# Performance work log

Measured on AMD Instinct MI355X. Metric: run time of the kernel, lower is better.

The kernel has to match this reference:

```python
import jax, jax.numpy as jnp
import numpy as np
import math

B, T, D, H = 8, 1024, 512, 8
DK = D // H


def setup_inputs() -> dict:
    key = jax.random.key(0)
    ks = jax.random.split(key, 16)
    f = lambda k, s: jax.random.normal(k, s, dtype=jnp.float32)
    p = lambda k, s: jax.random.normal(k, s, dtype=jnp.float32) * 0.02
    return {
        "query": f(ks[0], (B, T, D)),
        "key": f(ks[1], (B, T, D)),
        "value": f(ks[2], (B, T, D)),
        "pos_embedding": f(ks[3], (B, T, D)),
        "Wq": p(ks[4], (D, D)), "bq": p(ks[5], (D,)),
        "Wk": p(ks[6], (D, D)), "bk": p(ks[7], (D,)),
        "Wv": p(ks[8], (D, D)), "bv": p(ks[9], (D,)),
        "Wp": p(ks[10], (D, D)),
        "u_bias": p(ks[11], (H, DK)),
        "v_bias": p(ks[12], (H, DK)),
        "Wo": p(ks[13], (D, D)), "bo": p(ks[14], (D,)),
    }


def _rel_shift(pos_score):
    # pos_score: [B, H, T, T]  -> Transformer-XL relative shift via pad/reshape
    b, h, t1, t2 = pos_score.shape
    padded = jnp.concatenate(
        [jnp.zeros((b, h, t1, 1), pos_score.dtype), pos_score], axis=-1
    )  # [B,H,T,T+1]
    padded = padded.reshape(b, h, t2 + 1, t1)
    return padded[:, :, 1:].reshape(b, h, t1, t2)


def reference(query, key, value, pos_embedding, Wq, bq, Wk, bk, Wv, bv, Wp,
              u_bias, v_bias, Wo, bo):
    q = (query @ Wq + bq).reshape(B, T, H, DK)          # [B,T,H,DK]
    k = (key @ Wk + bk).reshape(B, T, H, DK)
    v = (value @ Wv + bv).reshape(B, T, H, DK)
    p = (pos_embedding @ Wp).reshape(B, T, H, DK)

    content_score = jnp.einsum("bihd,bjhd->bhij", q + u_bias, k)
    pos_score = jnp.einsum("bihd,bjhd->bhij", q + v_bias, p)
    pos_score = _rel_shift(pos_score)

    score = (content_score + pos_score) / math.sqrt(D)  # note: sqrt(d_model)
    attn = jax.nn.softmax(score, axis=-1)               # dropout: eval mode
    context = jnp.einsum("bhij,bjhd->bihd", attn, v).reshape(B, T, D)
    return context @ Wo + bo
```

## Files before the change

### kernel.cpp

```cpp
#include <hip/hip_runtime.h>

#define B_ 8
#define T_ 1024
#define D_ 512
#define H_ 8
#define DK_ 64

typedef __bf16 bf16x8 __attribute__((ext_vector_type(8)));
typedef float f32x4 __attribute__((ext_vector_type(4)));

#define MFMA16(a, b, c) __builtin_amdgcn_mfma_f32_16x16x32_bf16(a, b, c, 0, 0, 0)

__device__ __forceinline__ bf16x8 pack8(float4 a, float4 b) {
  bf16x8 r;
  r[0] = (__bf16)a.x; r[1] = (__bf16)a.y; r[2] = (__bf16)a.z; r[3] = (__bf16)a.w;
  r[4] = (__bf16)b.x; r[5] = (__bf16)b.y; r[6] = (__bf16)b.z; r[7] = (__bf16)b.w;
  return r;
}

__device__ __forceinline__ void load_lds16(const void* g, void* l) {
  __builtin_amdgcn_global_load_lds(
      (const __attribute__((address_space(1))) void*)g,
      (__attribute__((address_space(3))) void*)l, 16, 0, 0);
}

__global__ __launch_bounds__(256) void cvt_w(const float* __restrict__ w0,
                                             const float* __restrict__ w1,
                                             const float* __restrict__ w2,
                                             const float* __restrict__ w3,
                                             const float* __restrict__ w4,
                                             __bf16* __restrict__ wt) {
  __shared__ float Ts[64][65];
  const float* W = (blockIdx.z == 0) ? w0
                 : (blockIdx.z == 1) ? w1
                 : (blockIdx.z == 2) ? w2
                 : (blockIdx.z == 3) ? w3 : w4;
  const int tid = threadIdx.x;
  const int kt = blockIdx.x * 64, nt = blockIdx.y * 64;
  const int r = tid >> 2, co = (tid & 3) * 16;
#pragma unroll
  for (int q = 0; q < 4; ++q)
    *(float4*)&Ts[r][co + q * 4] =
        *(const float4*)(W + (size_t)(kt + r) * 512 + nt + co + q * 4);
  __syncthreads();
  bf16x8 o0, o1;
#pragma unroll
  for (int q = 0; q < 8; ++q) o0[q] = (__bf16)Ts[co + q][r];
#pragma unroll
  for (int q = 0; q < 8; ++q) o1[q] = (__bf16)Ts[co + 8 + q][r];
  const int key = r & 7;
  __bf16* dst =
      wt + (size_t)blockIdx.z * 262144 + (size_t)(nt + r) * 512 + kt;
  *(bf16x8*)(dst + (((co >> 3) ^ key) << 3)) = o0;
  *(bf16x8*)(dst + ((((co >> 3) + 1) ^ key) << 3)) = o1;
}

template <int PHASE>
__global__ __launch_bounds__(256, 4) void gemm_dma(
    const float* __restrict__ qf, const float* __restrict__ kf,
    const float* __restrict__ vf, const float* __restrict__ pf,
    const __bf16* __restrict__ ctxA, const __bf16* __restrict__ Wt,
    const float* __restrict__ bq, const float* __restrict__ bk,
    const float* __restrict__ bv, const float* __restrict__ bo,
    const float* __restrict__ ub, const float* __restrict__ vb,
    __bf16* __restrict__ quB, __bf16* __restrict__ qvB,
    __bf16* __restrict__ kB, __bf16* __restrict__ vT,
    __bf16* __restrict__ pB, float* __restrict__ out) {
  __shared__ __bf16 smem[17408];
  __bf16* As = smem;
  __bf16* Bs = smem + 8192;
  const int tid = threadIdx.x;
  const int z = blockIdx.z;
  const int wave = tid >> 6, lane = tid & 63, l16 = lane & 15, quad = lane >> 4;
  const int wm = wave & 1, wn = wave >> 1;
  const int m0 = blockIdx.x * 128, n0 = blockIdx.y * 128;

  const float* Af = (z == 0) ? qf : (z == 1) ? kf : (z == 2) ? vf : pf;
  const __bf16* Bg = Wt + (size_t)(PHASE ? 4 : z) * (512 * 512);

  const int drow = tid >> 3, dch = (tid & 7) * 8;
  char* ldsA = (char*)As + (tid & 192) * 16;
  char* ldsB = (char*)Bs + (tid & 192) * 16;
  const int keyc = l16 & 7;

  f32x4 acc[4][4];
#pragma unroll
  for (int rb = 0; rb < 4; ++rb)
#pragma unroll
    for (int cb = 0; cb < 4; ++cb) acc[rb][cb] = 0.f;

#pragma unroll 1
  for (int k0 = 0; k0 < 512; k0 += 64) {
    __syncthreads();
#pragma unroll
    for (int c4 = 0; c4 < 4; ++c4)
      load_lds16(Bg + (size_t)(n0 + c4 * 32 + drow) * 512 + k0 + dch,
                 ldsB + c4 * 4096);
    if (PHASE == 1) {
#pragma unroll
      for (int c4 = 0; c4 < 4; ++c4)
        load_lds16(ctxA + (size_t)(m0 + c4 * 32 + drow) * 512 + k0 + dch,
                   ldsA + c4 * 4096);
    } else {
#pragma unroll
      for (int c4 = 0; c4 < 4; ++c4) {
        const int row = c4 * 32 + drow;
        const float* s = Af + (size_t)(m0 + row) * 512 + k0 + dch;
        float4 a0 = *(const float4*)s;
        float4 a1 = *(const float4*)(s + 4);
        *(bf16x8*)&As[row * 64 + ((((dch >> 3) ^ row) & 7) << 3)] =
            pack8(a0, a1);
      }
    }
    __syncthreads();
#pragma unroll
    for (int s = 0; s < 2; ++s) {
      const int ph = ((s * 4 + quad) ^ keyc) << 3;
      bf16x8 afr[4], bfr[4];
#pragma unroll
      for (int rb = 0; rb < 4; ++rb)
        afr[rb] = *(const bf16x8*)&As[(wm * 64 + rb * 16 + l16) * 64 + ph];
#pragma unroll
      for (int cb = 0; cb < 4; ++cb)
        bfr[cb] = *(const bf16x8*)&Bs[(wn * 64 + cb * 16 + l16) * 64 + ph];
#pragma unroll
      for (int rb = 0; rb < 4; ++rb)
#pragma unroll
        for (int cb = 0; cb < 4; ++cb)
          acc[rb][cb] = MFMA16(afr[rb], bfr[cb], acc[rb][cb]);
    }
  }

  if (PHASE == 1) {
#pragma unroll
    for (int rb = 0; rb < 4; ++rb)
#pragma unroll
      for (int cb = 0; cb < 4; ++cb) {
        const int col = n0 + wn * 64 + cb * 16 + l16;
        const float bb = bo[col];
#pragma unroll
        for (int r = 0; r < 4; ++r) {
          const int row = m0 + wm * 64 + rb * 16 + quad * 4 + r;
          out[(size_t)row * 512 + col] = acc[rb][cb][r] + bb;
        }
      }
    return;
  }

  __syncthreads();

  if (z == 2) {
    __bf16* Tt = smem;
#pragma unroll
    for (int rb = 0; rb < 4; ++rb)
#pragma unroll
      for (int cb = 0; cb < 4; ++cb) {
        const int cl = wn * 64 + cb * 16 + l16;
        const float bb = bv[n0 + cl];
#pragma unroll
        for (int r = 0; r < 4; ++r) {
          const int rl = wm * 64 + rb * 16 + quad * 4 + r;
          Tt[cl * 136 + rl] = (__bf16)(acc[rb][cb][r] + bb);
        }
      }
    __syncthreads();
    const int r2 = tid >> 1, ch = (tid & 1) * 64;
    const int hh = (n0 + r2) >> 6, dkk = (n0 + r2) & 63;
    const int bI = m0 >> 10, t0 = m0 & 1023;
    __bf16* dst = vT + (((size_t)(bI * H_ + hh)) * DK_ + dkk) * T_ + t0 + ch;
    const int vkey = dkk & 7;
#pragma unroll
    for (int q = 0; q < 8; ++q)
      *(bf16x8*)(dst + ((q ^ vkey) * 8)) =
          *(const bf16x8*)&Tt[r2 * 136 + ch + q * 8];
    return;
  }

  __bf16* Tt = smem;
  const int trow = tid & 127, hs = tid >> 7;
  const int bI = m0 >> 10, tt = (m0 & 1023) + trow;
  const int hh = (n0 >> 6) + hs;
  const size_t obase = (((size_t)(bI * H_ + hh)) * T_ + tt) * DK_;
  const int npass = (z == 0) ? 2 : 1;
#pragma unroll 1
  for (int pass = 0; pass < npass; ++pass) {
#pragma unroll
    for (int rb = 0; rb < 4; ++rb)
#pragma unroll
      for (int cb = 0; cb < 4; ++cb) {
        const int cl = wn * 64 + cb * 16 + l16;
        const int col = n0 + cl;
        const float b0 = (z == 0) ? bq[col] : (z == 1) ? bk[col] : 0.f;
        const float b1 = (z == 0) ? (pass ? vb[col] : ub[col]) : 0.f;
#pragma unroll
        for (int r = 0; r < 4; ++r) {
          const int rl = wm * 64 + rb * 16 + quad * 4 + r;
          Tt[rl * 136 + cl] = (__bf16)((acc[rb][cb][r] + b0) + b1);
        }
      }
    __syncthreads();
    __bf16* dst = ((z == 0) ? (pass ? qvB : quB) : (z == 1) ? kB : pB) + obase;
#pragma unroll
    for (int qd = 0; qd < 8; ++qd) {
      const int c = (z == 0) ? qd : (qd ^ (tt & 7));
      *(bf16x8*)(dst + c * 8) =
          *(const bf16x8*)&Tt[trow * 136 + hs * 64 + qd * 8];
    }
    if (pass + 1 < npass) __syncthreads();
  }
}

__global__ __launch_bounds__(256, 4) void attn_mfma(
    const __bf16* __restrict__ qu, const __bf16* __restrict__ qv,
    const __bf16* __restrict__ kbuf, const __bf16* __restrict__ vT,
    const __bf16* __restrict__ pbuf, __bf16* __restrict__ ctx) {
  constexpr float SCALE = 0.044194173824159216f;
  __shared__ __bf16 smemA[4488];
  __shared__ __bf16 Vt[4096];
  __shared__ __bf16 Pb[8192];
  __bf16* Kt = smemA;
  __bf16* Rs = smemA;
  __bf16* Pa = Pb;

  const int tid = threadIdx.x;
  const int wave = tid >> 6, lane = tid & 63, l16 = lane & 15, quad = lane >> 4;
  const int g = blockIdx.x;
  const int bhq = (g & 7) * 8 + (g >> 7);
  const int i0 = ((g >> 3) & 15) * 64;
  const size_t bh = (size_t)bhq * T_ * DK_;
  const __bf16* QU = qu + bh;
  const __bf16* QV = qv + bh;
  const __bf16* Kg = kbuf + bh;
  const __bf16* Vg = vT + bh;
  const __bf16* Pg = pbuf + bh;

  bf16x8 quA[2], qvw[2], qv4[2];
  {
    const int rw = i0 + wave * 16 + l16;
    const int r4g = i0 + 64 + l16;
    const int r4 = (r4g < T_) ? r4g : T_ - 1;
#pragma unroll
    for (int s = 0; s < 2; ++s) {
      const int ko = s * 32 + quad * 8;
      quA[s] = *(const bf16x8*)&QU[(size_t)rw * DK_ + ko];
      qvw[s] = *(const bf16x8*)&QV[(size_t)rw * DK_ + ko];
      qv4[s] = *(const bf16x8*)&QV[(size_t)r4 * DK_ + ko];
    }
  }

  f32x4 Oacc[4];
#pragma unroll
  for (int cb = 0; cb < 4; ++cb) Oacc[cb] = 0.f;
  float lrun[4];
#pragma unroll
  for (int r = 0; r < 4; ++r) lrun[r] = 0.f;

  const int rbase = wave * 16 + quad * 4;
  const int keyr = l16 & 7;
  const int keyp = (l16 + 7) & 7;
  const int drow = tid >> 3;
  const int dch = (tid & 7) * 8;
  char* ldsK = (char*)Kt + (tid & 192) * 16;
  char* ldsV = (char*)Vt + (tid & 192) * 16;
  char* ldsP = (char*)Pb + (tid & 192) * 16;

#pragma unroll 1
  for (int jt = 0; jt < 16; ++jt) {
    const int j0 = jt * 64;
    int cs = T_ - 65 + j0 - i0;
    if (cs < 0) cs += T_;
    if (cs >= T_) cs -= T_;

    __syncthreads();
    load_lds16(Kg + (size_t)(j0 + drow) * 64 + dch, ldsK);
    load_lds16(Kg + (size_t)(j0 + 32 + drow) * 64 + dch, ldsK + 4096);
    __builtin_amdgcn_sched_barrier(0);
    load_lds16(Vg + (size_t)drow * T_ + j0 + dch, ldsV);
    load_lds16(Vg + (size_t)(32 + drow) * T_ + j0 + dch, ldsV + 4096);
#pragma unroll
    for (int c = 0; c < 4; ++c) {
      int prow = cs + c * 32 + drow;
      if (prow >= T_) prow -= T_;
      load_lds16(Pg + (size_t)prow * 64 + dch, ldsP + c * 4096);
    }
    asm volatile("s_waitcnt vmcnt(6)" ::: "memory");
    __builtin_amdgcn_s_barrier();

    f32x4 sA[4];
#pragma unroll
    for (int cb = 0; cb < 4; ++cb) sA[cb] = 0.f;
#pragma unroll
    for (int s = 0; s < 2; ++s)
#pragma unroll
      for (int cb = 0; cb < 4; ++cb) {
        bf16x8 kf = *(const bf16x8*)&Kt[(cb * 16 + l16) * 64 +
                                        (((s * 4 + quad) ^ keyr) << 3)];
        sA[cb] = MFMA16(quA[s], kf, sA[cb]);
      }

    asm volatile("s_waitcnt vmcnt(0)" ::: "memory");
    __builtin_amdgcn_s_barrier();

#pragma unroll
    for (int c = 0; c < 5; ++c) {
      const int cb = 3 - wave + c;
      f32x4 rc = 0.f;
#pragma unroll
      for (int s = 0; s < 2; ++s) {
        bf16x8 pf = *(const bf16x8*)&Pb[(cb * 16 + l16) * 64 +
                                        (((s * 4 + quad) ^ keyp) << 3)];
        rc = MFMA16(qvw[s], pf, rc);
      }
      const int col = cb * 16 + l16;
#pragma unroll
      for (int rr = 0; rr < 4; ++rr) {
        const int dj = col + rbase + rr - 64;
        if (dj >= 0 && dj < 64) Rs[(rbase + rr) * 68 + dj] = (__bf16)rc[rr];
      }
    }
    {
      const int cb = wave;
      f32x4 rc = 0.f;
#pragma unroll
      for (int s = 0; s < 2; ++s) {
        bf16x8 pf = *(const bf16x8*)&Pb[(cb * 16 + l16) * 64 +
                                        (((s * 4 + quad) ^ keyp) << 3)];
        rc = MFMA16(qv4[s], pf, rc);
      }
      if (quad == 0) Rs[64 * 68 + cb * 16 + l16] = (__bf16)rc[0];
    }
    __syncthreads();

#pragma unroll
    for (int r = 0; r < 4; ++r) {
#pragma unroll
      for (int cb = 0; cb < 4; ++cb) {
        const int di = rbase + r;
        const int dj = cb * 16 + l16;
        const int ji = (j0 + dj) - (i0 + di);
        float pos = 0.f;
        if (ji != 1) pos = (float)Rs[(di + (ji >= 2 ? 1 : 0)) * 68 + dj];
        const float w_ = __expf((sA[cb][r] + pos) * SCALE);
        lrun[r] += w_;
        Pa[di * 64 + (dj & 7) + ((((dj >> 3) ^ di) & 7) << 3)] = (__bf16)w_;
      }
    }

#pragma unroll
    for (int s = 0; s < 2; ++s) {
      bf16x8 ap = *(const bf16x8*)&Pa[(wave * 16 + l16) * 64 +
                                      (((s * 4 + quad) ^ keyr) << 3)];
#pragma unroll
      for (int cb = 0; cb < 4; ++cb) {
        bf16x8 bv = *(const bf16x8*)&Vt[(cb * 16 + l16) * 64 +
                                        (((s * 4 + quad) ^ keyr) << 3)];
        Oacc[cb] = MFMA16(ap, bv, Oacc[cb]);
      }
    }
  }

  float inv[4];
#pragma unroll
  for (int r = 0; r < 4; ++r) {
    float L = lrun[r];
    L += __shfl_xor(L, 1);
    L += __shfl_xor(L, 2);
    L += __shfl_xor(L, 4);
    L += __shfl_xor(L, 8);
    inv[r] = 1.f / L;
  }
  const int b = bhq >> 3, h = bhq & 7;
#pragma unroll
  for (int cb = 0; cb < 4; ++cb)
#pragma unroll
    for (int r = 0; r < 4; ++r) {
      const int row = i0 + rbase + r;
      const int chunk = cb * 2 + (l16 >> 3);
      const int col = h * DK_ + ((chunk ^ (row & 7)) << 3) + (l16 & 7);
      ctx[((size_t)(b * T_ + row)) * D_ + col] = (__bf16)(Oacc[cb][r] * inv[r]);
    }
}

extern "C" void kernel_launch(void* const* d_in, const int* in_sizes, int n_in,
                              void* d_out, int out_size, void* d_ws,
                              size_t ws_size, hipStream_t stream) {
  const float* query = (const float*)d_in[0];
  const float* key   = (const float*)d_in[1];
  const float* value = (const float*)d_in[2];
  const float* pos   = (const float*)d_in[3];
  const float* Wq = (const float*)d_in[4];
  const float* bq = (const float*)d_in[5];
  const float* Wk = (const float*)d_in[6];
  const float* bk = (const float*)d_in[7];
  const float* Wv = (const float*)d_in[8];
  const float* bv = (const float*)d_in[9];
  const float* Wp = (const float*)d_in[10];
  const float* ub = (const float*)d_in[11];
  const float* vbias = (const float*)d_in[12];
  const float* Wo = (const float*)d_in[13];
  const float* bo = (const float*)d_in[14];
  float* out = (float*)d_out;

  char* ws = (char*)d_ws;
  const size_t ACT = (size_t)8192 * 512 * 2;
  __bf16* quB = (__bf16*)ws;
  __bf16* qvB = (__bf16*)(ws + 1 * ACT);
  __bf16* kB  = (__bf16*)(ws + 2 * ACT);
  __bf16* pB  = (__bf16*)(ws + 3 * ACT);
  __bf16* vT  = (__bf16*)(ws + 4 * ACT);
  __bf16* ctx = (__bf16*)(ws + 5 * ACT);
  __bf16* Wt  = (__bf16*)(ws + 6 * ACT);

  cvt_w<<<dim3(8, 8, 5), 256, 0, stream>>>(Wq, Wk, Wv, Wp, Wo, Wt);

  gemm_dma<0><<<dim3(64, 4, 4), 256, 0, stream>>>(
      query, key, value, pos, nullptr, Wt, bq, bk, bv, bo, ub, vbias,
      quB, qvB, kB, vT, pB, nullptr);

  attn_mfma<<<dim3(1024), 256, 0, stream>>>(quB, qvB, kB, vT, pB, ctx);

  gemm_dma<1><<<dim3(64, 4, 1), 256, 0, stream>>>(
      nullptr, nullptr, nullptr, nullptr, ctx, Wt, bq, bk, bv, bo, ub, vbias,
      quB, qvB, kB, vT, pB, out);
}
```

Before: 247.1 us.

## Double-buffer LDS tiles in projection GEMM to overlap loads with MFMA

Converts the projection/output GEMM main loop to a two-stage LDS double buffer. The next K-tile's global loads (DMA into LDS for weights and ctx, registers for the fp32 activations) are issued before the current tile's MFMAs and written afterwards, which removes one barrier per iteration. This is meant to hide global load latency behind compute. LDS use doubles to 64KB and the launch-bounds occupancy hint drops from 4 to 2, so fewer blocks can be resident per CU.

```diff
diff --git a/kernel.cpp b/kernel.cpp
--- a/kernel.cpp
+++ b/kernel.cpp
@@ -56,7 +56,7 @@
 }
 
 template <int PHASE>
-__global__ __launch_bounds__(256, 4) void gemm_dma(
+__global__ __launch_bounds__(256, 2) void gemm_dma(
     const float* __restrict__ qf, const float* __restrict__ kf,
     const float* __restrict__ vf, const float* __restrict__ pf,
     const __bf16* __restrict__ ctxA, const __bf16* __restrict__ Wt,
@@ -66,9 +66,9 @@
     __bf16* __restrict__ quB, __bf16* __restrict__ qvB,
     __bf16* __restrict__ kB, __bf16* __restrict__ vT,
     __bf16* __restrict__ pB, float* __restrict__ out) {
-  __shared__ __bf16 smem[17408];
+  __shared__ __bf16 smem[32768];
   __bf16* As = smem;
-  __bf16* Bs = smem + 8192;
+  __bf16* Bs = smem + 16384;
   const int tid = threadIdx.x;
   const int z = blockIdx.z;
   const int wave = tid >> 6, lane = tid & 63, l16 = lane & 15, quad = lane >> 4;
@@ -89,46 +89,72 @@
 #pragma unroll
     for (int cb = 0; cb < 4; ++cb) acc[rb][cb] = 0.f;
 
+  float4 pa[4][2];
+
+#define STAGE_ISSUE(KK, BUF)                                                  \
+  {                                                                           \
+    if (PHASE == 1) {                                                         \
+      _Pragma("unroll") for (int c4 = 0; c4 < 4; ++c4)                        \
+          load_lds16(ctxA + (size_t)(m0 + c4 * 32 + drow) * 512 + (KK) + dch, \
+                     ldsA + (BUF) * 16384 + c4 * 4096);                       \
+    } else {                                                                  \
+      _Pragma("unroll") for (int c4 = 0; c4 < 4; ++c4) {                      \
+        const float* s_ =                                                     \
+            Af + (size_t)(m0 + c4 * 32 + drow) * 512 + (KK) + dch;            \
+        pa[c4][0] = *(const float4*)s_;                                       \
+        pa[c4][1] = *(const float4*)(s_ + 4);                                 \
+      }                                                                       \
+    }                                                                         \
+    _Pragma("unroll") for (int c4 = 0; c4 < 4; ++c4)                          \
+        load_lds16(Bg + (size_t)(n0 + c4 * 32 + drow) * 512 + (KK) + dch,     \
+                   ldsB + (BUF) * 16384 + c4 * 4096);                         \
+  }
+
+#define STAGE_WRITE(BUF)                                                      \
+  {                                                                           \
+    if (PHASE == 0) {                                                         \
+      _Pragma("unroll") for (int c4 = 0; c4 < 4; ++c4) {                      \
+        const int row_ = c4 * 32 + drow;                                      \
+        *(bf16x8*)&As[(BUF) * 8192 + row_ * 64 +                              \
+                      ((((dch >> 3) ^ row_) & 7) << 3)] =                     \
+            pack8(pa[c4][0], pa[c4][1]);                                      \
+      }                                                                       \
+    }                                                                         \
+  }
+
+  int cur = 0;
+  STAGE_ISSUE(0, 0)
+  STAGE_WRITE(0)
+  __syncthreads();
+
 #pragma unroll 1
   for (int k0 = 0; k0 < 512; k0 += 64) {
-    __syncthreads();
-#pragma unroll
-    for (int c4 = 0; c4 < 4; ++c4)
-      load_lds16(Bg + (size_t)(n0 + c4 * 32 + drow) * 512 + k0 + dch,
-                 ldsB + c4 * 4096);
-    if (PHASE == 1) {
-#pragma unroll
-      for (int c4 = 0; c4 < 4; ++c4)
-        load_lds16(ctxA + (size_t)(m0 + c4 * 32 + drow) * 512 + k0 + dch,
-                   ldsA + c4 * 4096);
-    } else {
-#pragma unroll
-      for (int c4 = 0; c4 < 4; ++c4) {
-        const int row = c4 * 32 + drow;
-        const float* s = Af + (size_t)(m0 + row) * 512 + k0 + dch;
-        float4 a0 = *(const float4*)s;
-        float4 a1 = *(const float4*)(s + 4);
-        *(bf16x8*)&As[row * 64 + ((((dch >> 3) ^ row) & 7) << 3)] =
-            pack8(a0, a1);
-      }
-    }
-    __syncthreads();
+    const int nxt = cur ^ 1;
+    if (k0 + 64 < 512) STAGE_ISSUE(k0 + 64, nxt)
+    __builtin_amdgcn_sched_barrier(0);
+
+    const __bf16* Asr = As + cur * 8192;
+    const __bf16* Bsr = Bs + cur * 8192;
 #pragma unroll
     for (int s = 0; s < 2; ++s) {
       const int ph = ((s * 4 + quad) ^ keyc) << 3;
       bf16x8 afr[4], bfr[4];
 #pragma unroll
       for (int rb = 0; rb < 4; ++rb)
-        afr[rb] = *(const bf16x8*)&As[(wm * 64 + rb * 16 + l16) * 64 + ph];
+        afr[rb] = *(const bf16x8*)&Asr[(wm * 64 + rb * 16 + l16) * 64 + ph];
 #pragma unroll
       for (int cb = 0; cb < 4; ++cb)
-        bfr[cb] = *(const bf16x8*)&Bs[(wn * 64 + cb * 16 + l16) * 64 + ph];
+        bfr[cb] = *(const bf16x8*)&Bsr[(wn * 64 + cb * 16 + l16) * 64 + ph];
 #pragma unroll
       for (int rb = 0; rb < 4; ++rb)
 #pragma unroll
         for (int cb = 0; cb < 4; ++cb)
           acc[rb][cb] = MFMA16(afr[rb], bfr[cb], acc[rb][cb]);
     }
+    __builtin_amdgcn_sched_barrier(0);
+    if (k0 + 64 < 512) STAGE_WRITE(nxt)
+    __syncthreads();
+    cur = nxt;
   }
 
   if (PHASE == 1) {
@@ -146,8 +172,6 @@
       }
     return;
   }
-
-  __syncthreads();
 
   if (z == 2) {
     __bf16* Tt = smem;
```

Result: no change. 247.4 us (+0.1%).

## Use 512-thread GEMM blocks, head-major context layout, and reuse buffers

Applied to the files above, without the earlier changes.

The projection GEMM now runs 512 threads (8 waves) per 128x128 tile, with each wave owning a 64x32 sub-tile. This halves per-thread accumulators to raise occupancy. The attention kernel now writes context in a per-head [B,H,T,DK] layout into the quB buffer in place, and the output GEMM gathers A tiles from that layout. K and P intermediates move into the output buffer, which shrinks the workspace and may improve cache locality. The risk is aliasing: quB is overwritten while other blocks may still be reading it, and d_out is reused before the final GEMM writes to it.

```diff
diff --git a/kernel.cpp b/kernel.cpp
--- a/kernel.cpp
+++ b/kernel.cpp
@@ -56,10 +56,10 @@
 }
 
 template <int PHASE>
-__global__ __launch_bounds__(256, 4) void gemm_dma(
+__global__ __launch_bounds__(512, 6) void gemm_dma(
     const float* __restrict__ qf, const float* __restrict__ kf,
     const float* __restrict__ vf, const float* __restrict__ pf,
-    const __bf16* __restrict__ ctxA, const __bf16* __restrict__ Wt,
+    const __bf16* __restrict__ ctxq, const __bf16* __restrict__ Wt,
     const float* __restrict__ bq, const float* __restrict__ bk,
     const float* __restrict__ bv, const float* __restrict__ bo,
     const float* __restrict__ ub, const float* __restrict__ vb,
@@ -79,54 +79,56 @@
   const __bf16* Bg = Wt + (size_t)(PHASE ? 4 : z) * (512 * 512);
 
   const int drow = tid >> 3, dch = (tid & 7) * 8;
-  char* ldsA = (char*)As + (tid & 192) * 16;
-  char* ldsB = (char*)Bs + (tid & 192) * 16;
+  char* ldsA = (char*)As + ((tid & 448) << 4);
+  char* ldsB = (char*)Bs + ((tid & 448) << 4);
   const int keyc = l16 & 7;
-
-  f32x4 acc[4][4];
+  const int arow = tid >> 2, af0 = (tid & 3) * 16;
+  const int ac0 = af0 >> 3;
+
+  f32x4 acc[4][2];
 #pragma unroll
   for (int rb = 0; rb < 4; ++rb)
 #pragma unroll
-    for (int cb = 0; cb < 4; ++cb) acc[rb][cb] = 0.f;
+    for (int cb = 0; cb < 2; ++cb) acc[rb][cb] = 0.f;
 
 #pragma unroll 1
   for (int k0 = 0; k0 < 512; k0 += 64) {
     __syncthreads();
-#pragma unroll
-    for (int c4 = 0; c4 < 4; ++c4)
-      load_lds16(Bg + (size_t)(n0 + c4 * 32 + drow) * 512 + k0 + dch,
-                 ldsB + c4 * 4096);
+    load_lds16(Bg + (size_t)(n0 + drow) * 512 + k0 + dch, ldsB);
+    load_lds16(Bg + (size_t)(n0 + 64 + drow) * 512 + k0 + dch, ldsB + 8192);
     if (PHASE == 1) {
-#pragma unroll
-      for (int c4 = 0; c4 < 4; ++c4)
-        load_lds16(ctxA + (size_t)(m0 + c4 * 32 + drow) * 512 + k0 + dch,
-                   ldsA + c4 * 4096);
+      const int h1 = k0 >> 6;
+      const int g0 = m0 + drow, g1 = m0 + 64 + drow;
+      load_lds16(ctxq + (((size_t)((g0 >> 10) * 8 + h1)) * 1024 + (g0 & 1023)) *
+                            64 + dch,
+                 ldsA);
+      load_lds16(ctxq + (((size_t)((g1 >> 10) * 8 + h1)) * 1024 + (g1 & 1023)) *
+                            64 + dch,
+                 ldsA + 8192);
     } else {
-#pragma unroll
-      for (int c4 = 0; c4 < 4; ++c4) {
-        const int row = c4 * 32 + drow;
-        const float* s = Af + (size_t)(m0 + row) * 512 + k0 + dch;
-        float4 a0 = *(const float4*)s;
-        float4 a1 = *(const float4*)(s + 4);
-        *(bf16x8*)&As[row * 64 + ((((dch >> 3) ^ row) & 7) << 3)] =
-            pack8(a0, a1);
-      }
+      const float* s = Af + (size_t)(m0 + arow) * 512 + k0 + af0;
+      float4 a0 = *(const float4*)s;
+      float4 a1 = *(const float4*)(s + 4);
+      float4 a2 = *(const float4*)(s + 8);
+      float4 a3 = *(const float4*)(s + 12);
+      *(bf16x8*)&As[arow * 64 + ((ac0 ^ (arow & 7)) << 3)] = pack8(a0, a1);
+      *(bf16x8*)&As[arow * 64 + (((ac0 + 1) ^ (arow & 7)) << 3)] = pack8(a2, a3);
     }
     __syncthreads();
 #pragma unroll
     for (int s = 0; s < 2; ++s) {
       const int ph = ((s * 4 + quad) ^ keyc) << 3;
-      bf16x8 afr[4], bfr[4];
+      bf16x8 afr[4], bfr[2];
 #pragma unroll
       for (int rb = 0; rb < 4; ++rb)
         afr[rb] = *(const bf16x8*)&As[(wm * 64 + rb * 16 + l16) * 64 + ph];
 #pragma unroll
-      for (int cb = 0; cb < 4; ++cb)
-        bfr[cb] = *(const bf16x8*)&Bs[(wn * 64 + cb * 16 + l16) * 64 + ph];
+      for (int cb = 0; cb < 2; ++cb)
+        bfr[cb] = *(const bf16x8*)&Bs[(wn * 32 + cb * 16 + l16) * 64 + ph];
 #pragma unroll
       for (int rb = 0; rb < 4; ++rb)
 #pragma unroll
-        for (int cb = 0; cb < 4; ++cb)
+        for (int cb = 0; cb < 2; ++cb)
           acc[rb][cb] = MFMA16(afr[rb], bfr[cb], acc[rb][cb]);
     }
   }
@@ -135,8 +137,8 @@
 #pragma unroll
     for (int rb = 0; rb < 4; ++rb)
 #pragma unroll
-      for (int cb = 0; cb < 4; ++cb) {
-        const int col = n0 + wn * 64 + cb * 16 + l16;
+      for (int cb = 0; cb < 2; ++cb) {
+        const int col = n0 + wn * 32 + cb * 16 + l16;
         const float bb = bo[col];
 #pragma unroll
         for (int r = 0; r < 4; ++r) {
@@ -154,8 +156,8 @@
 #pragma unroll
     for (int rb = 0; rb < 4; ++rb)
 #pragma unroll
-      for (int cb = 0; cb < 4; ++cb) {
-        const int cl = wn * 64 + cb * 16 + l16;
+      for (int cb = 0; cb < 2; ++cb) {
+        const int cl = wn * 32 + cb * 16 + l16;
         const float bb = bv[n0 + cl];
 #pragma unroll
         for (int r = 0; r < 4; ++r) {
@@ -164,22 +166,29 @@
         }
       }
     __syncthreads();
-    const int r2 = tid >> 1, ch = (tid & 1) * 64;
+    const int r2 = tid >> 2;
+    const int tseg = (tid & 3) >> 1;
+    const int qb = (tid & 1) * 4;
     const int hh = (n0 + r2) >> 6, dkk = (n0 + r2) & 63;
     const int bI = m0 >> 10, t0 = m0 & 1023;
-    __bf16* dst = vT + (((size_t)(bI * H_ + hh)) * DK_ + dkk) * T_ + t0 + ch;
+    __bf16* dst =
+        vT + (((size_t)(bI * H_ + hh)) * DK_ + dkk) * T_ + t0 + tseg * 64;
     const int vkey = dkk & 7;
 #pragma unroll
-    for (int q = 0; q < 8; ++q)
-      *(bf16x8*)(dst + ((q ^ vkey) * 8)) =
-          *(const bf16x8*)&Tt[r2 * 136 + ch + q * 8];
+    for (int q = 0; q < 4; ++q) {
+      const int gq = qb + q;
+      *(bf16x8*)(dst + ((gq ^ vkey) * 8)) =
+          *(const bf16x8*)&Tt[r2 * 136 + tseg * 64 + gq * 8];
+    }
     return;
   }
 
   __bf16* Tt = smem;
-  const int trow = tid & 127, hs = tid >> 7;
+  const int trow = tid >> 2;
+  const int cseg = tid & 3;
   const int bI = m0 >> 10, tt = (m0 & 1023) + trow;
-  const int hh = (n0 >> 6) + hs;
+  const int hh = (n0 >> 6) + (cseg >> 1);
+  const int gqb = (cseg & 1) * 4;
   const size_t obase = (((size_t)(bI * H_ + hh)) * T_ + tt) * DK_;
   const int npass = (z == 0) ? 2 : 1;
 #pragma unroll 1
@@ -187,8 +196,8 @@
 #pragma unroll
     for (int rb = 0; rb < 4; ++rb)
 #pragma unroll
-      for (int cb = 0; cb < 4; ++cb) {
-        const int cl = wn * 64 + cb * 16 + l16;
+      for (int cb = 0; cb < 2; ++cb) {
+        const int cl = wn * 32 + cb * 16 + l16;
         const int col = n0 + cl;
         const float b0 = (z == 0) ? bq[col] : (z == 1) ? bk[col] : 0.f;
         const float b1 = (z == 0) ? (pass ? vb[col] : ub[col]) : 0.f;
@@ -201,10 +210,11 @@
     __syncthreads();
     __bf16* dst = ((z == 0) ? (pass ? qvB : quB) : (z == 1) ? kB : pB) + obase;
 #pragma unroll
-    for (int qd = 0; qd < 8; ++qd) {
-      const int c = (z == 0) ? qd : (qd ^ (tt & 7));
+    for (int q = 0; q < 4; ++q) {
+      const int gq = gqb + q;
+      const int c = (z == 0) ? gq : (gq ^ (tt & 7));
       *(bf16x8*)(dst + c * 8) =
-          *(const bf16x8*)&Tt[trow * 136 + hs * 64 + qd * 8];
+          *(const bf16x8*)&Tt[trow * 136 + cseg * 32 + q * 8];
     }
     if (pass + 1 < npass) __syncthreads();
   }
@@ -369,15 +379,14 @@
     L += __shfl_xor(L, 8);
     inv[r] = 1.f / L;
   }
-  const int b = bhq >> 3, h = bhq & 7;
 #pragma unroll
   for (int cb = 0; cb < 4; ++cb)
 #pragma unroll
     for (int r = 0; r < 4; ++r) {
       const int row = i0 + rbase + r;
       const int chunk = cb * 2 + (l16 >> 3);
-      const int col = h * DK_ + ((chunk ^ (row & 7)) << 3) + (l16 & 7);
-      ctx[((size_t)(b * T_ + row)) * D_ + col] = (__bf16)(Oacc[cb][r] * inv[r]);
+      const int colin = ((chunk ^ (row & 7)) << 3) + (l16 & 7);
+      ctx[bh + (size_t)row * DK_ + colin] = (__bf16)(Oacc[cb][r] * inv[r]);
     }
 }
 
@@ -405,21 +414,20 @@
   const size_t ACT = (size_t)8192 * 512 * 2;
   __bf16* quB = (__bf16*)ws;
   __bf16* qvB = (__bf16*)(ws + 1 * ACT);
-  __bf16* kB  = (__bf16*)(ws + 2 * ACT);
-  __bf16* pB  = (__bf16*)(ws + 3 * ACT);
-  __bf16* vT  = (__bf16*)(ws + 4 * ACT);
-  __bf16* ctx = (__bf16*)(ws + 5 * ACT);
-  __bf16* Wt  = (__bf16*)(ws + 6 * ACT);
+  __bf16* vT  = (__bf16*)(ws + 2 * ACT);
+  __bf16* Wt  = (__bf16*)(ws + 3 * ACT);
+  __bf16* kB  = (__bf16*)d_out;
+  __bf16* pB  = (__bf16*)((char*)d_out + ACT);
 
   cvt_w<<<dim3(8, 8, 5), 256, 0, stream>>>(Wq, Wk, Wv, Wp, Wo, Wt);
 
-  gemm_dma<0><<<dim3(64, 4, 4), 256, 0, stream>>>(
+  gemm_dma<0><<<dim3(64, 4, 4), 512, 0, stream>>>(
       query, key, value, pos, nullptr, Wt, bq, bk, bv, bo, ub, vbias,
       quB, qvB, kB, vT, pB, nullptr);
 
-  attn_mfma<<<dim3(1024), 256, 0, stream>>>(quB, qvB, kB, vT, pB, ctx);
-
-  gemm_dma<1><<<dim3(64, 4, 1), 256, 0, stream>>>(
-      nullptr, nullptr, nullptr, nullptr, ctx, Wt, bq, bk, bv, bo, ub, vbias,
+  attn_mfma<<<dim3(1024), 256, 0, stream>>>(quB, qvB, kB, vT, pB, quB);
+
+  gemm_dma<1><<<dim3(64, 4, 1), 512, 0, stream>>>(
+      nullptr, nullptr, nullptr, nullptr, quB, Wt, bq, bk, bv, bo, ub, vbias,
       quB, qvB, kB, vT, pB, out);
 }
```

Result: slower. 264.6 us (+7.1%).
